# Optimization experiments

Measured on AMD Instinct MI355X. Metric: run time of the kernel, lower is better.

## Reference

```python
import jax, jax.numpy as jnp
import numpy as np

T, B = 128, 256
C_IN, H = 1024, 1024


def setup_inputs() -> dict:
    key = jax.random.key(0)
    ks = jax.random.split(key, 6)
    x = jax.random.normal(ks[0], (T * B, C_IN), dtype=jnp.float32)
    Wi = jax.random.normal(ks[1], (C_IN, 4 * H), dtype=jnp.float32) / np.sqrt(C_IN)
    Wh = jax.random.normal(ks[2], (H, 4 * H), dtype=jnp.float32) / np.sqrt(H)
    b = jax.random.normal(ks[3], (4 * H,), dtype=jnp.float32) * 0.01
    done = jax.random.randint(ks[4], (T * B,), 0, 2) > 0
    main = jax.random.randint(ks[5], (T * B,), 0, 2) > 0
    zeros = jnp.zeros((B, H), dtype=jnp.float32)
    return {"x": x, "c1": zeros, "h1": zeros, "c2": zeros, "h2": zeros,
            "Wi": Wi, "Wh": Wh, "b": b, "done": done, "main": main}


def reference(x, c1, h1, c2, h2, Wi, Wh, b, done, main):
    batch = c1.shape[0]
    num_steps = x.shape[0] // batch
    x3 = x.reshape(num_steps, batch, -1)
    done3 = done.reshape(num_steps, batch)
    main3 = main.reshape(num_steps, batch)

    def step(carry, inp):
        (r1c, r1h), (r2c, r2h) = carry
        xt, dt, mt = inp
        m = mt[:, None]  # [B,1] select player-1 vs player-2 state
        c = jnp.where(m, r1c, r2c)
        h = jnp.where(m, r1h, r2h)
        # OptimizedLSTMCell: fused gates, flax order i, f, g, o
        z = xt @ Wi + h @ Wh + b
        i, f, g, o = jnp.split(z, 4, axis=-1)
        nc = jax.nn.sigmoid(f) * c + jax.nn.sigmoid(i) * jnp.tanh(g)
        nh = jax.nn.sigmoid(o) * jnp.tanh(nc)
        # write back only to the active player's state
        n1c = jnp.where(m, nc, r1c); n1h = jnp.where(m, nh, r1h)
        n2c = jnp.where(m, r2c, nc); n2h = jnp.where(m, r2h, nh)
        # reset both states where episode is done
        d = dt[:, None]
        n1c = jnp.where(d, 0.0, n1c); n1h = jnp.where(d, 0.0, n1h)
        n2c = jnp.where(d, 0.0, n2c); n2h = jnp.where(d, 0.0, n2h)
        return ((n1c, n1h), (n2c, n2h)), nh

    _, ys = jax.lax.scan(step, ((c1, h1), (c2, h2)), (x3, done3, main3))
    return ys.reshape(-1, ys.shape[-1])  # [T*B, H]
```

## Files before the change

### kernel.cpp

```cpp
#include <hip/hip_runtime.h>
#include <cstdint>
#include <cstddef>

typedef unsigned short u16;
typedef unsigned char u8;
typedef unsigned int u32;

typedef short s16x8 __attribute__((ext_vector_type(8)));
typedef float f32x4 __attribute__((ext_vector_type(4)));

#define MF(a,b,c) __builtin_amdgcn_mfma_f32_16x16x32_bf16((a),(b),(c),0,0,0)

__device__ __forceinline__ float b2f(u16 h){ u32 u = ((u32)h)<<16; float f; __builtin_memcpy(&f,&u,4); return f; }
__device__ __forceinline__ u16 f2b(float x){ u32 u; __builtin_memcpy(&u,&x,4); u += 0x7fffu + ((u>>16)&1u); return (u16)(u>>16); }
__device__ __forceinline__ u16 f2h(float x){ _Float16 h = (_Float16)x; u16 u; __builtin_memcpy(&u,&h,2); return u; }
__device__ __forceinline__ float h2f(u16 v){ _Float16 h; __builtin_memcpy(&h,&v,2); return (float)h; }
__device__ __forceinline__ float sigf(float x){ return __builtin_amdgcn_rcpf(1.f+__expf(-x)); }
__device__ __forceinline__ float tanh2(float x){
  float ax=fabsf(x); float e=__expf(-2.f*ax);
  float r=(1.f-e)*__builtin_amdgcn_rcpf(1.f+e);
  return x<0.f? -r : r;
}

typedef __attribute__((address_space(1))) const void gvoid_t;
typedef __attribute__((address_space(3))) void lvoid_t;
__device__ __forceinline__ void gl_lds16(const u16* src, u16* dst){
  __builtin_amdgcn_global_load_lds((gvoid_t*)src, (lvoid_t*)dst, 16, 0, 0);
}

__device__ __forceinline__ void st_u16_coh(u16* p, u16 v){
  asm volatile("global_store_short %0, %1, off sc0 sc1" :: "v"(p), "v"((u32)v) : "memory");
}
__device__ __forceinline__ void st_f32_coh(float* p, float v){
  asm volatile("global_store_dword %0, %1, off sc0 sc1" :: "v"(p), "v"(v) : "memory");
}
__device__ __forceinline__ s16x8 gload16(const u16* p){
  s16x8 r;
  asm volatile("global_load_dwordx4 %0, %1, off" : "=v"(r) : "v"(p) : "memory");
  return r;
}
__device__ __forceinline__ s16x8 gload16_coh(const u16* p){
  s16x8 r;
  asm volatile("global_load_dwordx4 %0, %1, off sc0 sc1" : "=v"(r) : "v"(p) : "memory");
  return r;
}

__global__ void detect_mask_mode(const u8* raw, int n, int* flag){
  __shared__ int cnt;
  int tid = threadIdx.x;
  if(tid==0) cnt=0;
  __syncthreads();
  int c=0;
  for(int i=tid;i<n;i+=blockDim.x) c += (raw[i]!=0);
  atomicAdd(&cnt, c);
  __syncthreads();
  if(tid==0) *flag = (cnt > (n>>2)) ? 1 : 0;
}

__global__ void convert_masks(const void* done_raw, const void* main_raw, u8* done_u8, u8* main_u8, int n, const int* flag){
  int mode = *flag;
  for(int i = blockIdx.x*blockDim.x + threadIdx.x; i<n; i += gridDim.x*blockDim.x){
    u8 d, m;
    if(mode){ d = ((const u8*)done_raw)[i]!=0; m = ((const u8*)main_raw)[i]!=0; }
    else    { d = ((const int*)done_raw)[i]!=0; m = ((const int*)main_raw)[i]!=0; }
    done_u8[i]=d; main_u8[i]=m;
  }
}

__global__ void zero_flags(int* p, int n){
  int i = threadIdx.x;
  if(i<n) p[i]=0;
}

__global__ void cvt_f32_bf16(const float* __restrict__ in, u16* __restrict__ out, int n4){
  int i = blockIdx.x*blockDim.x + threadIdx.x;
  if(i < n4){
    float4 v = ((const float4*)in)[i];
    ushort4 o;
    o.x=f2b(v.x); o.y=f2b(v.y); o.z=f2b(v.z); o.w=f2b(v.w);
    ((ushort4*)out)[i]=o;
  }
}

__global__ void transpose_to_bf16(const float* __restrict__ in, u16* __restrict__ out, int R, int C){
  __shared__ float tile[64][65];
  int c0 = blockIdx.x*64, r0 = blockIdx.y*64;
  int tx = threadIdx.x & 63, ty = threadIdx.x >> 6;
  for(int i=ty;i<64;i+=4) tile[i][tx] = in[(size_t)(r0+i)*C + c0 + tx];
  __syncthreads();
  for(int i=ty;i<64;i+=4) out[(size_t)(c0+i)*R + r0 + tx] = f2b(tile[tx][i]);
}

__global__ void init_hsel(const float* __restrict__ h1in, const float* __restrict__ h2in,
                          const u8* __restrict__ mmain, u16* __restrict__ hsel0){
  int i = blockIdx.x*blockDim.x + threadIdx.x;
  if(i < 256*1024){
    int row = i >> 10;
    hsel0[i] = f2b(mmain[row] ? h1in[i] : h2in[i]);
  }
}

__global__ __launch_bounds__(256) void gemm_zx(const u16* __restrict__ A, const u16* __restrict__ Bt,
                                               const float* __restrict__ bias, u16* __restrict__ C){
  __shared__ u16 As[128*32];
  __shared__ u16 Bs[128*32];
  const int nbx = 32;
  const int nwg = 8192;
  int gid = blockIdx.x;
  int per = nwg>>3;
  int g2 = (gid&7)*per + (gid>>3);
  int tpg = 8*nbx;
  int grp = g2/tpg, w = g2%tpg;
  int brow = grp*8 + (w & 7);
  int bcol = w >> 3;
  int row0 = brow<<7, col0 = bcol<<7;

  int tid=threadIdx.x, wid=tid>>6, lane=tid&63;
  int l15=lane&15, hi=lane>>4;
  int wm=(wid>>1)<<6, wn=(wid&1)<<6;

  f32x4 acc[4][4];
  #pragma unroll
  for(int m=0;m<4;m++)
    #pragma unroll
    for(int n=0;n<4;n++) acc[m][n]=(f32x4){0.f,0.f,0.f,0.f};

  for(int k0=0;k0<1024;k0+=32){
    __syncthreads();
    #pragma unroll
    for(int q=0;q<2;q++){
      int cb=q*256+wid*64;
      int ch=cb+lane;
      gl_lds16(A + (size_t)(row0+(ch>>2))*1024 + k0 + (ch&3)*8, &As[cb*8]);
    }
    #pragma unroll
    for(int q=0;q<2;q++){
      int cb=q*256+wid*64;
      int ch=cb+lane;
      gl_lds16(Bt + (size_t)(col0+(ch>>2))*1024 + k0 + (ch&3)*8, &Bs[cb*8]);
    }
    __syncthreads();
    s16x8 a[4], b[4];
    #pragma unroll
    for(int m=0;m<4;m++) a[m] = *(const s16x8*)&As[(wm+m*16+l15)*32 + hi*8];
    #pragma unroll
    for(int n=0;n<4;n++) b[n] = *(const s16x8*)&Bs[(wn+n*16+l15)*32 + hi*8];
    #pragma unroll
    for(int m=0;m<4;m++)
      #pragma unroll
      for(int n=0;n<4;n++)
        acc[m][n] = MF(a[m],b[n],acc[m][n]);
  }
  #pragma unroll
  for(int m=0;m<4;m++){
    #pragma unroll
    for(int n=0;n<4;n++){
      int c = col0+wn+n*16+l15;
      float bv = bias[c];
      #pragma unroll
      for(int j=0;j<4;j++){
        int r = row0+wm+m*16+hi*4+j;
        C[(size_t)r*4096+c] = f2h(acc[m][n][j] + bv);
      }
    }
  }
}

__global__ __launch_bounds__(512) __attribute__((amdgpu_waves_per_eu(2,2)))
void lstm_persist(
    const u16* __restrict__ Zx, const u16* __restrict__ Wht,
    u16* __restrict__ hs0, u16* __restrict__ hs1,
    const float* __restrict__ c1i, const float* __restrict__ h1i,
    const float* __restrict__ c2i, const float* __restrict__ h2i,
    const u8* __restrict__ mdone, const u8* __restrict__ mmain,
    float* __restrict__ out, int* __restrict__ ready)
{
  __shared__ u16 As[32768];
  __shared__ float zpart[4*2*32*33];

  const int bid = blockIdx.x;
  const int rg = bid & 7, jg = bid >> 3;
  const int r0 = rg << 5, j0 = jg << 5;
  const int tid = threadIdx.x, wid = tid >> 6, lane = tid & 63;
  const int l15 = lane & 15, hi = lane >> 4;
  const int gate = wid >> 1, kg = wid & 1;
  const int srow = tid >> 4, sc16 = tid & 15;
  const int erow = tid >> 5, ecol = tid & 31;

  s16x8 breg[2][16];
  {
    #pragma unroll
    for(int n=0;n<2;n++){
      const u16* wp = Wht + ((size_t)(gate*1024 + j0 + n*16 + l15))*1024 + kg*512 + hi*8;
      #pragma unroll
      for(int kk=0;kk<16;kk++) breg[n][kk] = gload16(wp + kk*32);
    }
    asm volatile("s_waitcnt vmcnt(0)" ::: "memory");
    __builtin_amdgcn_sched_barrier(0);
  }

  float c1r[2],c2r[2],h1r[2],h2r[2];
  #pragma unroll
  for(int e=0;e<2;e++){
    size_t sidx = (size_t)(r0 + e*16 + erow)*1024 + j0 + ecol;
    c1r[e]=c1i[sidx]; c2r[e]=c2i[sidx]; h1r[e]=h1i[sidx]; h2r[e]=h2i[sidx];
  }

  int* flag = ready + rg*32;

  for(int t=0;t<128;t++){
    float zr[4][2]; u8 md[2], mm[2], mm2[2];
    #pragma unroll
    for(int e=0;e<2;e++){
      int gb = t*256 + r0 + e*16 + erow;
      size_t base = (size_t)gb*4096 + j0 + ecol;
      #pragma unroll
      for(int g=0; g<4; g++)
        zr[g][e] = h2f(Zx[base + g*1024]);
      md[e]=mdone[gb]; mm[e]=mmain[gb];
      mm2[e] = (t<127) ? mmain[gb+256] : (u8)0;
    }

    if(t>0 && tid==0){
      while(__hip_atomic_load(flag, __ATOMIC_RELAXED, __HIP_MEMORY_SCOPE_AGENT) < 32*t)
        __builtin_amdgcn_s_sleep(1);
    }
    __syncthreads();
    __builtin_amdgcn_sched_barrier(0);

    const u16* hin = (t&1) ? hs1 : hs0;
    u16* hout = (t&1) ? hs0 : hs1;

    {
      const u16* hrow = hin + (size_t)(r0+srow)*1024;
      s16x8 v[8];
      #pragma unroll
      for(int kc=0;kc<8;kc++) v[kc] = gload16_coh(hrow + (kc*16+sc16)*8);
      asm volatile("s_waitcnt vmcnt(4)" ::: "memory");
      #pragma unroll
      for(int kc=0;kc<4;kc++){
        int chunk = kc*16+sc16;
        *(s16x8*)&As[chunk*256 + ((srow ^ (chunk&7))<<3)] = v[kc];
      }
      asm volatile("s_waitcnt vmcnt(0)" ::: "memory");
      #pragma unroll
      for(int kc=4;kc<8;kc++){
        int chunk = kc*16+sc16;
        *(s16x8*)&As[chunk*256 + ((srow ^ (chunk&7))<<3)] = v[kc];
      }
    }
    __syncthreads();

    f32x4 acc[2][2];
    #pragma unroll
    for(int m=0;m<2;m++)
      #pragma unroll
      for(int n=0;n<2;n++) acc[m][n]=(f32x4){0.f,0.f,0.f,0.f};
    #pragma unroll
    for(int kk=0;kk<16;kk++){
      int c0 = (kg*16 + kk)*4 + hi;
      s16x8 a0 = *(const s16x8*)&As[c0*256 + ((l15      ^ (c0&7))<<3)];
      s16x8 a1 = *(const s16x8*)&As[c0*256 + (((16+l15) ^ (c0&7))<<3)];
      acc[0][0] = MF(a0, breg[0][kk], acc[0][0]);
      acc[0][1] = MF(a0, breg[1][kk], acc[0][1]);
      acc[1][0] = MF(a1, breg[0][kk], acc[1][0]);
      acc[1][1] = MF(a1, breg[1][kk], acc[1][1]);
    }

    #pragma unroll
    for(int m=0;m<2;m++)
      #pragma unroll
      for(int n=0;n<2;n++)
        #pragma unroll
        for(int j=0;j<4;j++){
          int row = m*16 + hi*4 + j;
          zpart[((gate*2+kg)*32 + row)*33 + n*16 + l15] = acc[m][n][j];
        }
    __syncthreads();

    float nhv[2];
    #pragma unroll
    for(int e=0;e<2;e++){
      int row = e*16 + erow;
      float zi  = zr[0][e] + zpart[((0)*32+row)*33 + ecol] + zpart[((1)*32+row)*33 + ecol];
      float zf_ = zr[1][e] + zpart[((2)*32+row)*33 + ecol] + zpart[((3)*32+row)*33 + ecol];
      float zg  = zr[2][e] + zpart[((4)*32+row)*33 + ecol] + zpart[((5)*32+row)*33 + ecol];
      float zo  = zr[3][e] + zpart[((6)*32+row)*33 + ecol] + zpart[((7)*32+row)*33 + ecol];
      bool m_ = mm[e]!=0, d_ = md[e]!=0;
      float co = m_ ? c1r[e] : c2r[e];
      float nc = sigf(zf_)*co + sigf(zi)*tanh2(zg);
      float nhx = sigf(zo)*tanh2(nc);
      nhv[e] = nhx;
      float n1c = m_?nc:c1r[e], n2c = m_?c2r[e]:nc;
      float n1h = m_?nhx:h1r[e], n2h = m_?h2r[e]:nhx;
      if(d_){ n1c=0.f; n2c=0.f; n1h=0.f; n2h=0.f; }
      c1r[e]=n1c; c2r[e]=n2c; h1r[e]=n1h; h2r[e]=n2h;
      if(t<127)
        st_u16_coh(&hout[(size_t)(r0+row)*1024 + j0 + ecol], f2b(mm2[e] ? n1h : n2h));
    }
    asm volatile("s_waitcnt vmcnt(0)" ::: "memory");
    __syncthreads();
    if(t<127 && tid==0)
      __hip_atomic_fetch_add(flag, 1, __ATOMIC_RELAXED, __HIP_MEMORY_SCOPE_AGENT);

    #pragma unroll
    for(int e=0;e<2;e++){
      int gb = t*256 + r0 + e*16 + erow;
      st_f32_coh(&out[(size_t)gb*1024 + j0 + ecol], nhv[e]);
    }
  }
}

extern "C" void kernel_launch(void* const* d_in, const int* in_sizes, int n_in,
                              void* d_out, int out_size, void* d_ws, size_t ws_size,
                              hipStream_t stream){
  const float* x   = (const float*)d_in[0];
  const float* c1i = (const float*)d_in[1];
  const float* h1i = (const float*)d_in[2];
  const float* c2i = (const float*)d_in[3];
  const float* h2i = (const float*)d_in[4];
  const float* Wi  = (const float*)d_in[5];
  const float* Wh  = (const float*)d_in[6];
  const float* bias= (const float*)d_in[7];
  const void* done_raw = d_in[8];
  const void* main_raw = d_in[9];
  float* out = (float*)d_out;

  char* ws = (char*)d_ws;
  size_t off=0;
  auto alloc=[&](size_t sz)->char*{ char* p = ws+off; off += (sz+255)&~(size_t)255; return p; };

  u16* xb   = (u16*)alloc(33554432ull*2);
  u16* WiT  = (u16*)alloc(4096ull*1024*2);
  u16* WhT  = (u16*)alloc(4096ull*1024*2);
  u16* hs0  = (u16*)alloc(262144ull*2);
  u16* hs1  = (u16*)alloc(262144ull*2);
  u8* dmask = (u8*)alloc(32768);
  u8* mmask = (u8*)alloc(32768);
  int* flag = (int*)alloc(256);
  int* ready= (int*)alloc(1024);
  u16* Zx   = (u16*)alloc(268435456ull);

  detect_mask_mode<<<1,256,0,stream>>>((const u8*)done_raw, 32768, flag);
  convert_masks<<<64,256,0,stream>>>(done_raw, main_raw, dmask, mmask, 32768, flag);
  cvt_f32_bf16<<<32768,256,0,stream>>>(x, xb, 8388608);
  transpose_to_bf16<<<dim3(64,16),256,0,stream>>>(Wi, WiT, 1024, 4096);
  transpose_to_bf16<<<dim3(64,16),256,0,stream>>>(Wh, WhT, 1024, 4096);
  init_hsel<<<1024,256,0,stream>>>(h1i, h2i, mmask, hs0);
  zero_flags<<<1,256,0,stream>>>(ready, 256);

  gemm_zx<<<8192,256,0,stream>>>(xb, WiT, bias, Zx);

  lstm_persist<<<256,512,0,stream>>>(Zx,WhT,hs0,hs1,c1i,h1i,c2i,h2i,dmask,mmask,out,ready);
}
```

Before: 1.035 ms.

## Rewrite input-projection GEMM with 256x256 tiles, 4-stage LDS pipeline and swizzle

The x@Wi GEMM now uses 512-thread workgroups with 256x256 output tiles and a 4-deep ring of LDS buffers filled by asynchronous global-to-LDS loads. It waits with explicit vmcnt counts so that loads for later K steps overlap the MFMA work on the current one, and it XOR-swizzles the LDS layout to avoid bank conflicts. The larger tile raises data reuse per load and cuts the workgroup count from 8192 to 2048. In exchange it needs 128 KB of LDS and many more accumulator registers, and it depends on hand-counted waitcnt values being correct.

```diff
diff --git a/kernel.cpp b/kernel.cpp
--- a/kernel.cpp
+++ b/kernel.cpp
@@ -68,7 +68,7 @@
 }
 
 __global__ void zero_flags(int* p, int n){
-  int i = threadIdx.x;
+  int i = blockIdx.x*blockDim.x + threadIdx.x;
   if(i<n) p[i]=0;
 }
 
@@ -100,12 +100,13 @@
   }
 }
 
-__global__ __launch_bounds__(256) void gemm_zx(const u16* __restrict__ A, const u16* __restrict__ Bt,
-                                               const float* __restrict__ bias, u16* __restrict__ C){
-  __shared__ u16 As[128*32];
-  __shared__ u16 Bs[128*32];
-  const int nbx = 32;
-  const int nwg = 8192;
+__global__ __launch_bounds__(512) __attribute__((amdgpu_waves_per_eu(2,2)))
+void gemm_zx(const u16* __restrict__ A, const u16* __restrict__ Bt,
+             const float* __restrict__ bias, u16* __restrict__ C){
+  __shared__ u16 As[32768];
+  __shared__ u16 Bs[32768];
+  const int nbx = 16;
+  const int nwg = 2048;
   int gid = blockIdx.x;
   int per = nwg>>3;
   int g2 = (gid&7)*per + (gid>>3);
@@ -113,54 +114,83 @@
   int grp = g2/tpg, w = g2%tpg;
   int brow = grp*8 + (w & 7);
   int bcol = w >> 3;
-  int row0 = brow<<7, col0 = bcol<<7;
+  int row0 = brow<<8, col0 = bcol<<8;
 
   int tid=threadIdx.x, wid=tid>>6, lane=tid&63;
   int l15=lane&15, hi=lane>>4;
-  int wm=(wid>>1)<<6, wn=(wid&1)<<6;
-
-  f32x4 acc[4][4];
+  int wm=(wid>>2)<<7;
+  int wn=(wid&3)<<6;
+
+  int fsw = (l15>>1)&3;
+  u32 aoff = (u32)((wm + l15)*64 + ((hi ^ fsw)<<4));
+  u32 boff = (u32)((wn + l15)*64 + ((hi ^ fsw)<<4));
+
+  f32x4 acc[8][4];
   #pragma unroll
-  for(int m=0;m<4;m++)
+  for(int m=0;m<8;m++)
     #pragma unroll
     for(int n=0;n<4;n++) acc[m][n]=(f32x4){0.f,0.f,0.f,0.f};
 
-  for(int k0=0;k0<1024;k0+=32){
-    __syncthreads();
+  auto stage=[&](int kt){
+    int k0 = kt<<5;
+    int bo = (kt&3)<<13;
     #pragma unroll
     for(int q=0;q<2;q++){
-      int cb=q*256+wid*64;
-      int ch=cb+lane;
-      gl_lds16(A + (size_t)(row0+(ch>>2))*1024 + k0 + (ch&3)*8, &As[cb*8]);
+      int ch = q*512 + tid;
+      int r = ch>>2, p = ch&3;
+      int ks = p ^ ((r>>1)&3);
+      gl_lds16(A + (size_t)(row0+r)*1024 + k0 + ks*8, &As[bo + ch*8]);
     }
     #pragma unroll
     for(int q=0;q<2;q++){
-      int cb=q*256+wid*64;
-      int ch=cb+lane;
-      gl_lds16(Bt + (size_t)(col0+(ch>>2))*1024 + k0 + (ch&3)*8, &Bs[cb*8]);
-    }
-    __syncthreads();
-    s16x8 a[4], b[4];
-    #pragma unroll
-    for(int m=0;m<4;m++) a[m] = *(const s16x8*)&As[(wm+m*16+l15)*32 + hi*8];
-    #pragma unroll
-    for(int n=0;n<4;n++) b[n] = *(const s16x8*)&Bs[(wn+n*16+l15)*32 + hi*8];
-    #pragma unroll
-    for(int m=0;m<4;m++)
-      #pragma unroll
-      for(int n=0;n<4;n++)
-        acc[m][n] = MF(a[m],b[n],acc[m][n]);
-  }
+      int ch = q*512 + tid;
+      int r = ch>>2, p = ch&3;
+      int ks = p ^ ((r>>1)&3);
+      gl_lds16(Bt + (size_t)(col0+r)*1024 + k0 + ks*8, &Bs[bo + ch*8]);
+    }
+  };
+
+  stage(0); stage(1); stage(2);
+
+  #define GITER(KT, WAITSTR, DOISSUE) { \
+    asm volatile(WAITSTR ::: "memory"); \
+    __builtin_amdgcn_sched_barrier(0); \
+    __builtin_amdgcn_s_barrier(); \
+    __builtin_amdgcn_sched_barrier(0); \
+    if(DOISSUE) stage((KT)+3); \
+    const char* pa = (const char*)As + (((KT)&3)<<14); \
+    const char* pb = (const char*)Bs + (((KT)&3)<<14); \
+    s16x8 af[8], bf[4]; \
+    _Pragma("unroll") \
+    for(int m=0;m<8;m++) af[m] = *(const s16x8*)(pa + aoff + m*1024); \
+    _Pragma("unroll") \
+    for(int n=0;n<4;n++) bf[n] = *(const s16x8*)(pb + boff + n*1024); \
+    __builtin_amdgcn_s_setprio(1); \
+    _Pragma("unroll") \
+    for(int m=0;m<8;m++){ \
+      _Pragma("unroll") \
+      for(int n=0;n<4;n++) acc[m][n] = MF(af[m], bf[n], acc[m][n]); } \
+    __builtin_amdgcn_s_setprio(0); \
+  }
+
+  #pragma unroll 1
+  for(int kt=0; kt<30; kt++){
+    GITER(kt, "s_waitcnt vmcnt(8)", (kt<29))
+  }
+  GITER(30, "s_waitcnt vmcnt(4)", false)
+  GITER(31, "s_waitcnt vmcnt(0)", false)
+  #undef GITER
+
   #pragma unroll
-  for(int m=0;m<4;m++){
+  for(int m=0;m<8;m++){
     #pragma unroll
     for(int n=0;n<4;n++){
-      int c = col0+wn+n*16+l15;
+      int c = col0 + wn + n*16 + l15;
       float bv = bias[c];
       #pragma unroll
       for(int j=0;j<4;j++){
-        int r = row0+wm+m*16+hi*4+j;
-        C[(size_t)r*4096+c] = f2h(acc[m][n][j] + bv);
+        int r = row0 + wm + m*16 + hi*4 + j;
+        C[(size_t)r*4096 + c] = f2h(acc[m][n][j] + bv);
       }
     }
   }
@@ -349,7 +379,7 @@
   init_hsel<<<1024,256,0,stream>>>(h1i, h2i, mmask, hs0);
   zero_flags<<<1,256,0,stream>>>(ready, 256);
 
-  gemm_zx<<<8192,256,0,stream>>>(xb, WiT, bias, Zx);
+  gemm_zx<<<2048,512,0,stream>>>(xb, WiT, bias, Zx);
 
   lstm_persist<<<256,512,0,stream>>>(Zx,WhT,hs0,hs1,c1i,h1i,c2i,h2i,dmask,mmask,out,ready);
 }
```

Measured after the change: 1.054 ms. About the same (+1.9%).
